# Kernel optimization log

Hardware: AMD Instinct MI355X
Metric: run time of the kernel (lower is better)

## Reference

```python
import jax, jax.numpy as jnp
import numpy as np

B, L = 2, 160
RD = 128          # residue_dim
AD = 128          # atom_dim
NUM_AT = 37       # atom37
NSC = 34          # side-chain atom slots (37 - 3 backbone)
EPS = 8.0         # radius for eps_8 graph
NOISE = 0.5       # noise added to repeated CA positions
HID = 512         # decoder MLP hidden


def _precomputed_atom37_mask():
    # Stand-in for VALID_ATOM37_MASK [20 residue types, 37 atoms]:
    # backbone N,CA,C,O always present; deterministic pseudo side-chain counts.
    m = np.zeros((20, NUM_AT), np.float32)
    m[:, :4] = 1.0
    for r in range(20):
        nsc = 1 + (r * 7) % 10
        m[r, 4:4 + nsc] = 1.0
    return jnp.asarray(m)


def setup_inputs() -> dict:
    key = jax.random.key(0)
    ks = jax.random.split(key, 8)
    bb_pred = jax.random.normal(ks[0], (B, L, 3, 3), jnp.float32) * 10.0
    scalar_features = jax.random.normal(ks[1], (B, L, RD), jnp.float32)
    aa_pred = jax.random.normal(ks[2], (B, L, 20), jnp.float32)
    mask = jnp.ones((B, L), jnp.float32)
    residue_batch = jnp.repeat(jnp.arange(B, dtype=jnp.int64), L)
    # learned parameters
    atom_emb = jax.random.normal(ks[3], (NUM_AT, AD), jnp.float32) * 0.02
    W1 = jax.random.normal(ks[4], (2 * AD, HID), jnp.float32) / np.sqrt(2.0 * AD)
    b1 = jnp.zeros((HID,), jnp.float32)
    W2 = jax.random.normal(ks[5], (HID, 3), jnp.float32) / np.sqrt(float(HID))
    b2 = jnp.zeros((3,), jnp.float32)
    # pre-sampled position noise (torch.randn_like * noise)
    pos_noise = jax.random.normal(ks[6], (B, L, NSC, 3), jnp.float32) * NOISE
    precomputed_mask = _precomputed_atom37_mask()
    return dict(bb_pred=bb_pred, scalar_features=scalar_features, aa_pred=aa_pred,
                residue_batch=residue_batch, mask=mask, precomputed_mask=precomputed_mask,
                atom_emb=atom_emb, W1=W1, b1=b1, W2=W2, b2=b2, pos_noise=pos_noise)


def reference(bb_pred, scalar_features, aa_pred, residue_batch, mask,
              precomputed_mask, atom_emb, W1, b1, W2, b2, pos_noise):
    # --- generate_atom37_mask ---
    res_types = jnp.argmax(aa_pred, axis=-1)                       # [B,L]
    atom_mask = precomputed_mask[res_types] * mask[..., None]      # [B,L,37]

    # --- ResidueAndAtomEmbedder (dense, validity carried as mask) ---
    atom_type_emb = atom_emb[None, None] * atom_mask[..., None]    # [B,L,37,AD]
    combined = scalar_features[:, :, None, :] + atom_type_emb      # [B,L,37,AD]
    sc_mask = atom_mask[:, :, 3:]                                  # [B,L,34]
    h = combined[:, :, 3:, :] * sc_mask[..., None]                 # [B,L,34,AD]

    # --- reconstruct_edges: CA repeated per side-chain slot + noise ---
    ca = bb_pred[:, :, 1, :] * mask[..., None]                     # [B,L,3]
    pos = ca[:, :, None, :] + pos_noise                            # [B,L,34,3]

    Ns = L * NSC
    x = pos.reshape(B, Ns, 3)
    hf = h.reshape(B, Ns, AD)
    valid = sc_mask.reshape(B, Ns)                                 # batch axis B == residue_batch separation

    # pairwise squared distances [B,Ns,Ns] (eps_8 radius graph, dense masked form)
    x2 = jnp.sum(x * x, axis=-1)
    d2 = x2[:, :, None] + x2[:, None, :] - 2.0 * jnp.einsum('bnd,bmd->bnm', x, x)
    pair_valid = valid[:, :, None] * valid[:, None, :]
    w = jnp.where(d2 < EPS * EPS, jnp.exp(-d2 / (2.0 * EPS * EPS)), 0.0) * pair_valid

    # --- PositionDecoder (EGNN-style layer, self-loops contribute zero rel-pos) ---
    deg = jnp.sum(w, axis=-1, keepdims=True)                       # [B,Ns,1]
    inv = 1.0 / (deg + 1.0)
    agg_pos = (x * deg - jnp.einsum('bnm,bmd->bnd', w, x)) * inv   # sum_j w_ij (x_i - x_j), normalized
    h_agg = jnp.einsum('bnm,bmd->bnd', w, hf) * inv                # [B,Ns,AD]
    z = jnp.concatenate([hf, h_agg], axis=-1)                      # [B,Ns,2*AD]
    gate = jnp.tanh(jax.nn.relu(z @ W1 + b1) @ W2 + b2)            # [B,Ns,3]
    disp = agg_pos * gate * valid[..., None]

    updated_pos = (x + disp).reshape(B, L, NSC, 3)
    return atom_mask, updated_pos
```

## Files before the change

### kernel.cpp

```cpp
#include <hip/hip_runtime.h>
#include <hip/hip_bf16.h>
#include <math.h>

#define BB 2
#define LL 160
#define NSC 34
#define NS (LL * NSC)
#define TOT (BB * NS)
#define AD 128
#define ADX 144
#define HID 512
#define NAT 37
#define KC 4
#define NVP 1792
#define NVT 28
#define NVPT (BB * NVP)
#define PEN 1.0e9f

typedef __attribute__((ext_vector_type(4))) float f32x4;
typedef __attribute__((ext_vector_type(8))) short s16x8;
typedef __attribute__((address_space(1))) const unsigned int gu32;
typedef __attribute__((address_space(3))) unsigned int lu32;

__global__ __launch_bounds__(256) void k_pre(
    const float* __restrict__ W1, __hip_bfloat16* __restrict__ W1T,
    const float* __restrict__ bb, const float* __restrict__ aa,
    const float* __restrict__ mask, const float* __restrict__ pm,
    const float* __restrict__ noise,
    float* __restrict__ out_mask, float4* __restrict__ ws_xe,
    float* __restrict__ ws_val, float* __restrict__ out_pos) {
  __shared__ float t[64][65];
  int blk = blockIdx.x;
  int tid = threadIdx.x;
  if (blk < 32) {
    int j0 = (blk >> 2) * 64;
    int c0 = (blk & 3) * 64;
    for (int i = tid; i < 64 * 64; i += 256) {
      int jl = i & 63, cl = i >> 6;
      t[cl][jl] = W1[(size_t)(c0 + cl) * HID + j0 + jl];
    }
    __syncthreads();
    for (int i = tid; i < 64 * 64; i += 256) {
      int cl = i & 63, jl = i >> 6;
      W1T[(size_t)(j0 + jl) * 256 + c0 + cl] = __float2bfloat16(t[cl][jl]);
    }
    return;
  }
  int bl = blk - 32;
  int b = bl / LL, l = bl % LL;
  const float* ap = aa + bl * 20;
  float mv = ap[0]; int rt = 0;
  for (int r = 1; r < 20; ++r) { float v = ap[r]; if (v > mv) { mv = v; rt = r; } }
  float mk = mask[bl];
  const float* pmr = pm + rt * NAT;
  if (tid < NAT) out_mask[bl * NAT + tid] = pmr[tid] * mk;

  float ca0 = bb[(bl * 3 + 1) * 3 + 0] * mk;
  float ca1 = bb[(bl * 3 + 1) * 3 + 1] * mk;
  float ca2 = bb[(bl * 3 + 1) * 3 + 2] * mk;

  if (tid < NSC) {
    float am = pmr[3 + tid] * mk;
    const float* npz = noise + (bl * NSC + tid) * 3;
    float x = ca0 + npz[0], y = ca1 + npz[1], z = ca2 + npz[2];
    float4 xv;
    xv.x = x; xv.y = y; xv.z = z;
    xv.w = x * x + y * y + z * z + (am > 0.f ? 0.f : PEN);
    int g = b * NS + l * NSC + tid;
    ws_xe[g] = xv;
    ws_val[g] = am;
  }
  if (tid < NSC * 3) {
    int s = tid / 3, c = tid % 3;
    float ca = (c == 0) ? ca0 : (c == 1) ? ca1 : ca2;
    float pos = ca + noise[(bl * NSC + s) * 3 + c];
    out_pos[(size_t)(b * NS + l * NSC + s) * 3 + c] = pos;
  }
}

__global__ __launch_bounds__(256) void k_scan(
    const float* __restrict__ ws_val, const float4* __restrict__ ws_xe,
    int* __restrict__ cg2g, float4* __restrict__ xc) {
  __shared__ int scnt[256];
  __shared__ int sincl[256];
  __shared__ int smap[NVP];
  int b = blockIdx.x;
  int tid = threadIdx.x;
  int c = 0;
  if (tid < LL) {
    for (int s = 0; s < NSC; ++s)
      if (ws_val[b * NS + tid * NSC + s] > 0.f) ++c;
  }
  scnt[tid] = c;
  sincl[tid] = c;
  __syncthreads();
  #pragma unroll
  for (int off = 1; off < 256; off <<= 1) {
    int t = (tid >= off) ? sincl[tid - off] : 0;
    __syncthreads();
    sincl[tid] += t;
    __syncthreads();
  }
  for (int j = tid; j < NVP; j += 256) smap[j] = -1;
  __syncthreads();
  if (tid < LL) {
    int o = sincl[tid] - c, k = 0;
    for (int s = 0; s < NSC; ++s) {
      int m = tid * NSC + s;
      if (ws_val[b * NS + m] > 0.f) { smap[o + k] = m; ++k; }
    }
  }
  __syncthreads();
  for (int j = tid; j < NVP; j += 256) {
    int m = smap[j];
    cg2g[b * NVP + j] = m;
    float4 v;
    if (m >= 0) v = ws_xe[b * NS + m];
    else { v.x = 0.f; v.y = 0.f; v.z = 0.f; v.w = PEN; }
    xc[b * NVP + j] = v;
  }
}

__global__ __launch_bounds__(256) void k_prep1c(
    const float* __restrict__ sf, const float* __restrict__ emb,
    const float* __restrict__ ws_val, const int* __restrict__ cg2g,
    const float4* __restrict__ xc, __hip_bfloat16* __restrict__ hfTc,
    __hip_bfloat16* __restrict__ ws_z) {
  __shared__ __hip_bfloat16 tile[ADX][64];
  __shared__ int sm[64];
  int bid = blockIdx.x;
  int b = bid / NVT;
  int j0 = (bid % NVT) * 64;
  int tid = threadIdx.x;
  if (tid < 64) sm[tid] = cg2g[b * NVP + j0 + tid];
  __syncthreads();

  int jl = tid >> 2, cq = tid & 3;
  int m = sm[jl];
  union { s16x8 v[4]; __hip_bfloat16 h[32]; } o;
  if (m >= 0) {
    int l = m / NSC, s = m - l * NSC;
    float am = ws_val[b * NS + m];
    const float* sfp = sf + (size_t)(b * LL + l) * AD + cq * 32;
    const float* emp = emb + (size_t)(3 + s) * AD + cq * 32;
    #pragma unroll 8
    for (int k = 0; k < 32; ++k) {
      float hv = (sfp[k] + emp[k] * am) * am;
      o.h[k] = __float2bfloat16(hv);
      tile[cq * 32 + k][jl] = o.h[k];
    }
  } else {
    __hip_bfloat16 zz = __float2bfloat16(0.0f);
    #pragma unroll 8
    for (int k = 0; k < 32; ++k) { o.h[k] = zz; tile[cq * 32 + k][jl] = zz; }
  }
  {
    __hip_bfloat16* zp = ws_z + ((size_t)(b * NVP + j0 + jl)) * 128 + cq * 32;
    #pragma unroll
    for (int q = 0; q < 4; ++q) *(s16x8*)(zp + q * 8) = o.v[q];
  }
  if (cq == 0) {
    float4 xj = xc[b * NVP + j0 + jl];
    tile[128][jl] = __float2bfloat16(m >= 0 ? 1.0f : 0.0f);
    tile[129][jl] = __float2bfloat16(xj.x);
    tile[130][jl] = __float2bfloat16(xj.y);
    tile[131][jl] = __float2bfloat16(xj.z);
    __hip_bfloat16 zz = __float2bfloat16(0.0f);
    for (int rr = 132; rr < ADX; ++rr) tile[rr][jl] = zz;
  }
  __syncthreads();
  for (int i = tid; i < ADX * 2; i += 256) {
    int r = i >> 1, hf = i & 1;
    __hip_bfloat16* dst = hfTc + (size_t)b * ADX * NVP + (size_t)r * NVP + j0 + hf * 32;
    const __hip_bfloat16* srow = &tile[r][hf * 32];
    #pragma unroll
    for (int q = 0; q < 4; ++q)
      *(s16x8*)(dst + q * 8) = *(const s16x8*)(srow + q * 8);
  }
}

__global__ __launch_bounds__(256, 4) void k_haggc(
    const float4* __restrict__ xc, const __hip_bfloat16* __restrict__ hfTc,
    __hip_bfloat16* __restrict__ haggp, float* __restrict__ dgp) {
  constexpr int NSTEP = NVP / 32;
  constexpr int CH_MAX = (NSTEP + KC - 1) / KC;
  __shared__ float4 xs[(CH_MAX * 4 + 1) * 9];
  __shared__ alignas(16) __hip_bfloat16 sB[2][4608];

  int bid = blockIdx.x;
  int b = bid / (NVT * KC);
  int rem = bid % (NVT * KC);
  int kc = rem / NVT;
  int nt = rem % NVT;
  int n0 = nt * 64;
  int sb = (kc * NSTEP) / KC, se = ((kc + 1) * NSTEP) / KC;
  int tid = threadIdx.x, w = tid >> 6, lane = tid & 63;
  int ln = lane & 15, g8 = (lane >> 4) * 8;

  const float4* xb = xc + b * NVP;
  const __hip_bfloat16* hb = hfTc + (size_t)b * ADX * NVP;

  int mcnt = (se - sb) * 32;
  for (int i = tid; i < mcnt; i += 256)
    xs[(i >> 3) * 9 + (i & 7)] = xb[sb * 32 + i];

  float4 xn = xb[n0 + w * 16 + ln];
  float x2n = xn.w;

  f32x4 acc[9];
  #pragma unroll
  for (int ct = 0; ct < 9; ++ct) acc[ct] = (f32x4){0.f, 0.f, 0.f, 0.f};

  auto STAGE = [&](int s, int pb) {
    const char* srcb = (const char*)(hb + (size_t)s * 32);
    #pragma unroll
    for (int k = 0; k < 3; ++k) {
      int t = tid + k * 256;
      if (t < 576) {
        int row = t >> 2;
        int sl = (t & 3) ^ (row & 3);
        const gu32* gp = (const gu32*)(const void*)(srcb + (size_t)row * (NVP * 2) + sl * 16);
        lu32* lp = (lu32*)(void*)((char*)&sB[pb][0] + (size_t)(t & ~63) * 16);
        __builtin_amdgcn_global_load_lds(gp, lp, 16, 0, 0);
      }
    }
  };

  STAGE(sb, 0);
  __syncthreads();

  int cur = 0;
  for (int s = sb; s < se; ++s) {
    if (s + 1 < se) STAGE(s + 1, cur ^ 1);
    int grp = (s - sb) * 4 + (g8 >> 3);
    union { s16x8 v; __hip_bfloat16 h[8]; } af;
    #pragma unroll
    for (int j = 0; j < 8; ++j) {
      float4 xm = xs[grp * 9 + j];
      float dt = xn.x * xm.x + xn.y * xm.y + xn.z * xm.z;
      float d2 = x2n + xm.w - 2.f * dt;
      float wv = (d2 < 64.f) ? __expf(d2 * -0.0078125f) : 0.f;
      af.h[j] = __float2bfloat16(wv);
    }
    const char* bbase = (const char*)&sB[cur][0];
    int slot = g8 >> 3;
    #pragma unroll
    for (int ct = 0; ct < 9; ++ct) {
      int row = ct * 16 + ln;
      int boff = (row << 6) + ((slot ^ (row & 3)) << 4);
      s16x8 bf = *(const s16x8*)(bbase + boff);
      acc[ct] = __builtin_amdgcn_mfma_f32_16x16x32_bf16(af.v, bf, acc[ct], 0, 0, 0);
    }
    __syncthreads();
    cur ^= 1;
  }

  int q = lane >> 4;
  int grow = b * NVP + n0 + w * 16 + q * 4;
  #pragma unroll
  for (int ct = 0; ct < 8; ++ct)
    #pragma unroll
    for (int r = 0; r < 4; ++r)
      haggp[((size_t)kc * NVPT + grow + r) * AD + ct * 16 + ln] = __float2bfloat16(acc[ct][r]);
  if (ln < 4)
    #pragma unroll
    for (int r = 0; r < 4; ++r)
      dgp[((size_t)kc * NVPT + grow + r) * 4 + ln] = acc[8][r];
}

__global__ __launch_bounds__(512) void k_mlpf(
    const __hip_bfloat16* __restrict__ ws_z,
    const __hip_bfloat16* __restrict__ haggp, const float* __restrict__ dgp,
    const __hip_bfloat16* __restrict__ W1T, const float* __restrict__ b1v,
    const float* __restrict__ W2, const float* __restrict__ b2v,
    const float4* __restrict__ xc, const int* __restrict__ cg2g,
    const float* __restrict__ ws_val, float* __restrict__ out_pos) {
  __shared__ __hip_bfloat16 zt[32][136];
  __shared__ float sai[32][4];
  __shared__ float ppart[4][32][3];

  int r0 = blockIdx.x * 32;
  int tid = threadIdx.x, w = tid >> 6, lane = tid & 63;
  int ln = lane & 15, g8 = (lane >> 4) * 8, q = lane >> 4;
  int rowhalf = w & 1, js4 = w >> 1;

  if (tid < 32) {
    int g = r0 + tid;
    float deg = 0.f, wx = 0.f, wy = 0.f, wz = 0.f;
    #pragma unroll
    for (int kc = 0; kc < KC; ++kc) {
      float4 d = *(const float4*)&dgp[((size_t)kc * NVPT + g) * 4];
      deg += d.x; wx += d.y; wy += d.z; wz += d.w;
    }
    float inv = 1.f / (deg + 1.f);
    float4 xv = xc[g];
    sai[tid][0] = (xv.x * deg - wx) * inv;
    sai[tid][1] = (xv.y * deg - wy) * inv;
    sai[tid][2] = (xv.z * deg - wz) * inv;
    sai[tid][3] = inv;
  }
  __syncthreads();
  {
    int row = tid >> 4, c8 = tid & 15;
    int g = r0 + row;
    float s[8];
    #pragma unroll
    for (int j = 0; j < 8; ++j) s[j] = 0.f;
    #pragma unroll
    for (int kc = 0; kc < KC; ++kc) {
      union { s16x8 v; __hip_bfloat16 h[8]; } uu;
      uu.v = *(const s16x8*)(haggp + ((size_t)kc * NVPT + g) * AD + c8 * 8);
      #pragma unroll
      for (int j = 0; j < 8; ++j) s[j] += __bfloat162float(uu.h[j]);
    }
    float inv = sai[row][3];
    #pragma unroll
    for (int j = 0; j < 8; ++j)
      zt[row][c8 * 8 + j] = __float2bfloat16(s[j] * inv);
  }
  __syncthreads();

  int arl = rowhalf * 16 + ln;
  int arow = r0 + arl;
  s16x8 a[8];
  #pragma unroll
  for (int kq = 0; kq < 4; ++kq)
    a[kq] = *(const s16x8*)(ws_z + (size_t)arow * 128 + kq * 32 + g8);
  #pragma unroll
  for (int kq = 4; kq < 8; ++kq)
    a[kq] = *(const s16x8*)&zt[arl][(kq - 4) * 32 + g8];

  float p[4][3];
  #pragma unroll
  for (int r = 0; r < 4; ++r)
    #pragma unroll
    for (int o = 0; o < 3; ++o) p[r][o] = 0.f;

  #pragma unroll
  for (int jt = 0; jt < 8; ++jt) {
    int j = js4 * 128 + jt * 16 + ln;
    f32x4 acc = (f32x4){0.f, 0.f, 0.f, 0.f};
    #pragma unroll
    for (int kq = 0; kq < 8; ++kq) {
      s16x8 bw = *(const s16x8*)(W1T + (size_t)j * 256 + kq * 32 + g8);
      acc = __builtin_amdgcn_mfma_f32_16x16x32_bf16(a[kq], bw, acc, 0, 0, 0);
    }
    float bias = b1v[j];
    float w20 = W2[j * 3 + 0], w21 = W2[j * 3 + 1], w22 = W2[j * 3 + 2];
    #pragma unroll
    for (int r = 0; r < 4; ++r) {
      float h = fmaxf(acc[r] + bias, 0.f);
      p[r][0] += h * w20; p[r][1] += h * w21; p[r][2] += h * w22;
    }
  }
  #pragma unroll
  for (int r = 0; r < 4; ++r)
    #pragma unroll
    for (int o = 0; o < 3; ++o) {
      p[r][o] += __shfl_xor(p[r][o], 1);
      p[r][o] += __shfl_xor(p[r][o], 2);
      p[r][o] += __shfl_xor(p[r][o], 4);
      p[r][o] += __shfl_xor(p[r][o], 8);
    }
  if (ln == 0) {
    #pragma unroll
    for (int r = 0; r < 4; ++r) {
      int row = rowhalf * 16 + q * 4 + r;
      #pragma unroll
      for (int o = 0; o < 3; ++o) ppart[js4][row][o] = p[r][o];
    }
  }
  __syncthreads();

  if (tid < 32) {
    int row = tid;
    int g = r0 + row;
    int bq = g / NVP;
    int m = cg2g[g];
    if (m >= 0) {
      float p0 = b2v[0] + ppart[0][row][0] + ppart[1][row][0] + ppart[2][row][0] + ppart[3][row][0];
      float p1 = b2v[1] + ppart[0][row][1] + ppart[1][row][1] + ppart[2][row][1] + ppart[3][row][1];
      float p2 = b2v[2] + ppart[0][row][2] + ppart[1][row][2] + ppart[2][row][2] + ppart[3][row][2];
      float val = ws_val[bq * NS + m];
      float4 xv = xc[g];
      float* op = out_pos + (size_t)(bq * NS + m) * 3;
      op[0] = xv.x + sai[row][0] * tanhf(p0) * val;
      op[1] = xv.y + sai[row][1] * tanhf(p1) * val;
      op[2] = xv.z + sai[row][2] * tanhf(p2) * val;
    }
  }
}

extern "C" void kernel_launch(void* const* d_in, const int* in_sizes, int n_in,
                              void* d_out, int out_size, void* d_ws, size_t ws_size,
                              hipStream_t stream) {
  const float* bb    = (const float*)d_in[0];
  const float* sf    = (const float*)d_in[1];
  const float* aa    = (const float*)d_in[2];
  const float* mask  = (const float*)d_in[4];
  const float* pm    = (const float*)d_in[5];
  const float* emb   = (const float*)d_in[6];
  const float* W1    = (const float*)d_in[7];
  const float* b1v   = (const float*)d_in[8];
  const float* W2    = (const float*)d_in[9];
  const float* b2v   = (const float*)d_in[10];
  const float* noise = (const float*)d_in[11];

  float* out_mask = (float*)d_out;
  float* out_pos  = (float*)d_out + BB * LL * NAT;

  char* cur = (char*)d_ws;
  auto alloc = [&](size_t bytes) -> char* {
    char* p = cur;
    cur += (bytes + 15) & ~(size_t)15;
    return p;
  };
  float4* ws_xe  = (float4*)alloc((size_t)TOT * 16);
  float*  ws_val = (float*)alloc((size_t)TOT * 4);
  int*    cg2g   = (int*)alloc((size_t)BB * NVP * 4);
  float4* xc     = (float4*)alloc((size_t)BB * NVP * 16);
  float*  ws_dgp = (float*)alloc((size_t)KC * NVPT * 16);
  __hip_bfloat16* ws_w1t = (__hip_bfloat16*)alloc((size_t)HID * 256 * 2);
  __hip_bfloat16* hfTc   = (__hip_bfloat16*)alloc((size_t)BB * ADX * NVP * 2);
  __hip_bfloat16* haggp  = (__hip_bfloat16*)alloc((size_t)KC * NVPT * AD * 2);
  __hip_bfloat16* ws_z   = (__hip_bfloat16*)alloc((size_t)NVPT * 128 * 2);

  hipLaunchKernelGGL(k_pre, dim3(32 + BB * LL), dim3(256), 0, stream,
                     W1, ws_w1t, bb, aa, mask, pm, noise,
                     out_mask, ws_xe, ws_val, out_pos);
  hipLaunchKernelGGL(k_scan, dim3(BB), dim3(256), 0, stream,
                     ws_val, ws_xe, cg2g, xc);
  hipLaunchKernelGGL(k_prep1c, dim3(BB * NVT), dim3(256), 0, stream,
                     sf, emb, ws_val, cg2g, xc, hfTc, ws_z);
  hipLaunchKernelGGL(k_haggc, dim3(BB * NVT * KC), dim3(256), 0, stream,
                     xc, hfTc, haggp, ws_dgp);
  hipLaunchKernelGGL(k_mlpf, dim3(NVPT / 32), dim3(512), 0, stream,
                     ws_z, haggp, ws_dgp, ws_w1t, b1v, W2, b2v,
                     xc, cg2g, ws_val, out_pos);
}
```

Measured before the change: 58.90 us.

## Fuse five kernels into one persistent kernel with global grid barriers

```diff
diff --git a/kernel.cpp b/kernel.cpp
--- a/kernel.cpp
+++ b/kernel.cpp
@@ -15,6 +15,7 @@
 #define NVP 1792
 #define NVT 28
 #define NVPT (BB * NVP)
+#define NBLK 224
 #define PEN 1.0e9f
 
 typedef __attribute__((ext_vector_type(4))) float f32x4;
@@ -22,371 +23,374 @@
 typedef __attribute__((address_space(1))) const unsigned int gu32;
 typedef __attribute__((address_space(3))) unsigned int lu32;
 
-__global__ __launch_bounds__(256) void k_pre(
-    const float* __restrict__ W1, __hip_bfloat16* __restrict__ W1T,
-    const float* __restrict__ bb, const float* __restrict__ aa,
-    const float* __restrict__ mask, const float* __restrict__ pm,
-    const float* __restrict__ noise,
-    float* __restrict__ out_mask, float4* __restrict__ ws_xe,
-    float* __restrict__ ws_val, float* __restrict__ out_pos) {
-  __shared__ float t[64][65];
-  int blk = blockIdx.x;
+__device__ __forceinline__ void gbar(int* bar, int idx) {
+  __syncthreads();
+  if (threadIdx.x == 0) {
+    __threadfence();
+    int* cnt = bar + idx * 2;
+    int* flg = bar + idx * 2 + 1;
+    if (atomicAdd(cnt, 1) == NBLK - 1) {
+      atomicExch(flg, 1);
+    } else {
+      while (atomicAdd(flg, 0) == 0) __builtin_amdgcn_s_sleep(2);
+    }
+    __threadfence();
+  }
+  __syncthreads();
+}
+
+struct LdsP0 { float t[64][65]; };
+struct LdsP1 { int scnt[256]; int sincl[256]; int smap[NVP]; };
+struct LdsP2 { __hip_bfloat16 tile[ADX][64]; int sm[64]; };
+struct LdsP3 { float4 xs[57 * 9]; __hip_bfloat16 sB[2][4608]; };
+struct LdsP4 { __hip_bfloat16 zt[16][136]; float sai[16][4]; float ppart[4][16][3]; };
+
+__global__ __launch_bounds__(256) void k_mega(
+    const float* __restrict__ W1, const float* __restrict__ bb,
+    const float* __restrict__ aa, const float* __restrict__ mask,
+    const float* __restrict__ pm, const float* __restrict__ noise,
+    const float* __restrict__ sf, const float* __restrict__ emb,
+    const float* __restrict__ b1v, const float* __restrict__ W2,
+    const float* __restrict__ b2v,
+    float* __restrict__ out_mask, float* __restrict__ out_pos,
+    __hip_bfloat16* __restrict__ W1T, float4* __restrict__ ws_xe,
+    float* __restrict__ ws_val, int* __restrict__ cg2g,
+    float4* __restrict__ xc, __hip_bfloat16* __restrict__ hfTc,
+    __hip_bfloat16* __restrict__ ws_z, __hip_bfloat16* __restrict__ haggp,
+    float* __restrict__ dgp, int* bar) {
+  __shared__ union { LdsP0 p0; LdsP1 p1; LdsP2 p2; LdsP3 p3; LdsP4 p4; } u;
   int tid = threadIdx.x;
-  if (blk < 32) {
-    int j0 = (blk >> 2) * 64;
-    int c0 = (blk & 3) * 64;
-    for (int i = tid; i < 64 * 64; i += 256) {
-      int jl = i & 63, cl = i >> 6;
-      t[cl][jl] = W1[(size_t)(c0 + cl) * HID + j0 + jl];
-    }
-    __syncthreads();
-    for (int i = tid; i < 64 * 64; i += 256) {
-      int cl = i & 63, jl = i >> 6;
-      W1T[(size_t)(j0 + jl) * 256 + c0 + cl] = __float2bfloat16(t[cl][jl]);
-    }
-    return;
-  }
-  int bl = blk - 32;
-  int b = bl / LL, l = bl % LL;
-  const float* ap = aa + bl * 20;
-  float mv = ap[0]; int rt = 0;
-  for (int r = 1; r < 20; ++r) { float v = ap[r]; if (v > mv) { mv = v; rt = r; } }
-  float mk = mask[bl];
-  const float* pmr = pm + rt * NAT;
-  if (tid < NAT) out_mask[bl * NAT + tid] = pmr[tid] * mk;
-
-  float ca0 = bb[(bl * 3 + 1) * 3 + 0] * mk;
-  float ca1 = bb[(bl * 3 + 1) * 3 + 1] * mk;
-  float ca2 = bb[(bl * 3 + 1) * 3 + 2] * mk;
-
-  if (tid < NSC) {
-    float am = pmr[3 + tid] * mk;
-    const float* npz = noise + (bl * NSC + tid) * 3;
-    float x = ca0 + npz[0], y = ca1 + npz[1], z = ca2 + npz[2];
-    float4 xv;
-    xv.x = x; xv.y = y; xv.z = z;
-    xv.w = x * x + y * y + z * z + (am > 0.f ? 0.f : PEN);
-    int g = b * NS + l * NSC + tid;
-    ws_xe[g] = xv;
-    ws_val[g] = am;
-  }
-  if (tid < NSC * 3) {
-    int s = tid / 3, c = tid % 3;
-    float ca = (c == 0) ? ca0 : (c == 1) ? ca1 : ca2;
-    float pos = ca + noise[(bl * NSC + s) * 3 + c];
-    out_pos[(size_t)(b * NS + l * NSC + s) * 3 + c] = pos;
-  }
-}
-
-__global__ __launch_bounds__(256) void k_scan(
-    const float* __restrict__ ws_val, const float4* __restrict__ ws_xe,
-    int* __restrict__ cg2g, float4* __restrict__ xc) {
-  __shared__ int scnt[256];
-  __shared__ int sincl[256];
-  __shared__ int smap[NVP];
-  int b = blockIdx.x;
-  int tid = threadIdx.x;
-  int c = 0;
-  if (tid < LL) {
-    for (int s = 0; s < NSC; ++s)
-      if (ws_val[b * NS + tid * NSC + s] > 0.f) ++c;
-  }
-  scnt[tid] = c;
-  sincl[tid] = c;
-  __syncthreads();
-  #pragma unroll
-  for (int off = 1; off < 256; off <<= 1) {
-    int t = (tid >= off) ? sincl[tid - off] : 0;
-    __syncthreads();
-    sincl[tid] += t;
-    __syncthreads();
-  }
-  for (int j = tid; j < NVP; j += 256) smap[j] = -1;
-  __syncthreads();
-  if (tid < LL) {
-    int o = sincl[tid] - c, k = 0;
-    for (int s = 0; s < NSC; ++s) {
-      int m = tid * NSC + s;
-      if (ws_val[b * NS + m] > 0.f) { smap[o + k] = m; ++k; }
-    }
-  }
-  __syncthreads();
-  for (int j = tid; j < NVP; j += 256) {
-    int m = smap[j];
-    cg2g[b * NVP + j] = m;
-    float4 v;
-    if (m >= 0) v = ws_xe[b * NS + m];
-    else { v.x = 0.f; v.y = 0.f; v.z = 0.f; v.w = PEN; }
-    xc[b * NVP + j] = v;
-  }
-}
-
-__global__ __launch_bounds__(256) void k_prep1c(
-    const float* __restrict__ sf, const float* __restrict__ emb,
-    const float* __restrict__ ws_val, const int* __restrict__ cg2g,
-    const float4* __restrict__ xc, __hip_bfloat16* __restrict__ hfTc,
-    __hip_bfloat16* __restrict__ ws_z) {
-  __shared__ __hip_bfloat16 tile[ADX][64];
-  __shared__ int sm[64];
-  int bid = blockIdx.x;
-  int b = bid / NVT;
-  int j0 = (bid % NVT) * 64;
-  int tid = threadIdx.x;
-  if (tid < 64) sm[tid] = cg2g[b * NVP + j0 + tid];
-  __syncthreads();
-
-  int jl = tid >> 2, cq = tid & 3;
-  int m = sm[jl];
-  union { s16x8 v[4]; __hip_bfloat16 h[32]; } o;
-  if (m >= 0) {
-    int l = m / NSC, s = m - l * NSC;
-    float am = ws_val[b * NS + m];
-    const float* sfp = sf + (size_t)(b * LL + l) * AD + cq * 32;
-    const float* emp = emb + (size_t)(3 + s) * AD + cq * 32;
-    #pragma unroll 8
-    for (int k = 0; k < 32; ++k) {
-      float hv = (sfp[k] + emp[k] * am) * am;
-      o.h[k] = __float2bfloat16(hv);
-      tile[cq * 32 + k][jl] = o.h[k];
-    }
-  } else {
-    __hip_bfloat16 zz = __float2bfloat16(0.0f);
-    #pragma unroll 8
-    for (int k = 0; k < 32; ++k) { o.h[k] = zz; tile[cq * 32 + k][jl] = zz; }
-  }
+
+  for (int v = blockIdx.x; v < 32 + BB * LL; v += NBLK) {
+    if (v < 32) {
+      int j0 = (v >> 2) * 64, c0 = (v & 3) * 64;
+      for (int i = tid; i < 64 * 64; i += 256) {
+        int jl = i & 63, cl = i >> 6;
+        u.p0.t[cl][jl] = W1[(size_t)(c0 + cl) * HID + j0 + jl];
+      }
+      __syncthreads();
+      for (int i = tid; i < 64 * 64; i += 256) {
+        int cl = i & 63, jl = i >> 6;
+        W1T[(size_t)(j0 + jl) * 256 + c0 + cl] = __float2bfloat16(u.p0.t[cl][jl]);
+      }
+    } else {
+      int bl = v - 32;
+      int b = bl / LL, l = bl % LL;
+      const float* ap = aa + bl * 20;
+      float mv = ap[0]; int rt = 0;
+      for (int r = 1; r < 20; ++r) { float vv = ap[r]; if (vv > mv) { mv = vv; rt = r; } }
+      float mk = mask[bl];
+      const float* pmr = pm + rt * NAT;
+      if (tid < NAT) out_mask[bl * NAT + tid] = pmr[tid] * mk;
+
+      float ca0 = bb[(bl * 3 + 1) * 3 + 0] * mk;
+      float ca1 = bb[(bl * 3 + 1) * 3 + 1] * mk;
+      float ca2 = bb[(bl * 3 + 1) * 3 + 2] * mk;
+
+      if (tid < NSC) {
+        float am = pmr[3 + tid] * mk;
+        const float* npz = noise + (bl * NSC + tid) * 3;
+        float x = ca0 + npz[0], y = ca1 + npz[1], z = ca2 + npz[2];
+        float4 xv;
+        xv.x = x; xv.y = y; xv.z = z;
+        xv.w = x * x + y * y + z * z + (am > 0.f ? 0.f : PEN);
+        int g = b * NS + l * NSC + tid;
+        ws_xe[g] = xv;
+        ws_val[g] = am;
+      }
+      if (tid < NSC * 3) {
+        int s = tid / 3, c = tid % 3;
+        float ca = (c == 0) ? ca0 : (c == 1) ? ca1 : ca2;
+        float pos = ca + noise[(bl * NSC + s) * 3 + c];
+        out_pos[(size_t)(b * NS + l * NSC + s) * 3 + c] = pos;
+      }
+    }
+    __syncthreads();
+  }
+  gbar(bar, 0);
+
+  if (blockIdx.x < BB) {
+    int b = blockIdx.x;
+    int c = 0;
+    if (tid < LL) {
+      for (int s = 0; s < NSC; ++s)
+        if (ws_val[b * NS + tid * NSC + s] > 0.f) ++c;
+    }
+    u.p1.scnt[tid] = c;
+    u.p1.sincl[tid] = c;
+    __syncthreads();
+    #pragma unroll
+    for (int off = 1; off < 256; off <<= 1) {
+      int t = (tid >= off) ? u.p1.sincl[tid - off] : 0;
+      __syncthreads();
+      u.p1.sincl[tid] += t;
+      __syncthreads();
+    }
+    for (int j = tid; j < NVP; j += 256) u.p1.smap[j] = -1;
+    __syncthreads();
+    if (tid < LL) {
+      int o = u.p1.sincl[tid] - c, k = 0;
+      for (int s = 0; s < NSC; ++s) {
+        int m = tid * NSC + s;
+        if (ws_val[b * NS + m] > 0.f) { u.p1.smap[o + k] = m; ++k; }
+      }
+    }
+    __syncthreads();
+    for (int j = tid; j < NVP; j += 256) {
+      int m = u.p1.smap[j];
+      cg2g[b * NVP + j] = m;
+      float4 vv;
+      if (m >= 0) vv = ws_xe[b * NS + m];
+      else { vv.x = 0.f; vv.y = 0.f; vv.z = 0.f; vv.w = PEN; }
+      xc[b * NVP + j] = vv;
+    }
+  }
+  gbar(bar, 1);
+
+  if (blockIdx.x < BB * NVT) {
+    int bid = blockIdx.x;
+    int b = bid / NVT;
+    int j0 = (bid % NVT) * 64;
+    if (tid < 64) u.p2.sm[tid] = cg2g[b * NVP + j0 + tid];
+    __syncthreads();
+
+    int jl = tid >> 2, cq = tid & 3;
+    int m = u.p2.sm[jl];
+    union { s16x8 v[4]; __hip_bfloat16 h[32]; } o;
+    if (m >= 0) {
+      int l = m / NSC, s = m - l * NSC;
+      float am = ws_val[b * NS + m];
+      const float* sfp = sf + (size_t)(b * LL + l) * AD + cq * 32;
+      const float* emp = emb + (size_t)(3 + s) * AD + cq * 32;
+      #pragma unroll 8
+      for (int k = 0; k < 32; ++k) {
+        float hv = (sfp[k] + emp[k] * am) * am;
+        o.h[k] = __float2bfloat16(hv);
+        u.p2.tile[cq * 32 + k][jl] = o.h[k];
+      }
+    } else {
+      __hip_bfloat16 zz = __float2bfloat16(0.0f);
+      #pragma unroll 8
+      for (int k = 0; k < 32; ++k) { o.h[k] = zz; u.p2.tile[cq * 32 + k][jl] = zz; }
+    }
+    {
+      __hip_bfloat16* zp = ws_z + ((size_t)(b * NVP + j0 + jl)) * 128 + cq * 32;
+      #pragma unroll
+      for (int q = 0; q < 4; ++q) *(s16x8*)(zp + q * 8) = o.v[q];
+    }
+    if (cq == 0) {
+      float4 xj = xc[b * NVP + j0 + jl];
+      u.p2.tile[128][jl] = __float2bfloat16(m >= 0 ? 1.0f : 0.0f);
+      u.p2.tile[129][jl] = __float2bfloat16(xj.x);
+      u.p2.tile[130][jl] = __float2bfloat16(xj.y);
+      u.p2.tile[131][jl] = __float2bfloat16(xj.z);
+      __hip_bfloat16 zz = __float2bfloat16(0.0f);
+      for (int rr = 132; rr < ADX; ++rr) u.p2.tile[rr][jl] = zz;
+    }
+    __syncthreads();
+    for (int i = tid; i < ADX * 2; i += 256) {
+      int r = i >> 1, hf = i & 1;
+      __hip_bfloat16* dst = hfTc + (size_t)b * ADX * NVP + (size_t)r * NVP + j0 + hf * 32;
+      const __hip_bfloat16* srow = &u.p2.tile[r][hf * 32];
+      #pragma unroll
+      for (int q = 0; q < 4; ++q)
+        *(s16x8*)(dst + q * 8) = *(const s16x8*)(srow + q * 8);
+    }
+  }
+  gbar(bar, 2);
+
   {
-    __hip_bfloat16* zp = ws_z + ((size_t)(b * NVP + j0 + jl)) * 128 + cq * 32;
-    #pragma unroll
-    for (int q = 0; q < 4; ++q) *(s16x8*)(zp + q * 8) = o.v[q];
-  }
-  if (cq == 0) {
-    float4 xj = xc[b * NVP + j0 + jl];
-    tile[128][jl] = __float2bfloat16(m >= 0 ? 1.0f : 0.0f);
-    tile[129][jl] = __float2bfloat16(xj.x);
-    tile[130][jl] = __float2bfloat16(xj.y);
-    tile[131][jl] = __float2bfloat16(xj.z);
-    __hip_bfloat16 zz = __float2bfloat16(0.0f);
-    for (int rr = 132; rr < ADX; ++rr) tile[rr][jl] = zz;
-  }
-  __syncthreads();
-  for (int i = tid; i < ADX * 2; i += 256) {
-    int r = i >> 1, hf = i & 1;
-    __hip_bfloat16* dst = hfTc + (size_t)b * ADX * NVP + (size_t)r * NVP + j0 + hf * 32;
-    const __hip_bfloat16* srow = &tile[r][hf * 32];
-    #pragma unroll
-    for (int q = 0; q < 4; ++q)
-      *(s16x8*)(dst + q * 8) = *(const s16x8*)(srow + q * 8);
-  }
-}
-
-__global__ __launch_bounds__(256, 4) void k_haggc(
-    const float4* __restrict__ xc, const __hip_bfloat16* __restrict__ hfTc,
-    __hip_bfloat16* __restrict__ haggp, float* __restrict__ dgp) {
-  constexpr int NSTEP = NVP / 32;
-  constexpr int CH_MAX = (NSTEP + KC - 1) / KC;
-  __shared__ float4 xs[(CH_MAX * 4 + 1) * 9];
-  __shared__ alignas(16) __hip_bfloat16 sB[2][4608];
-
-  int bid = blockIdx.x;
-  int b = bid / (NVT * KC);
-  int rem = bid % (NVT * KC);
-  int kc = rem / NVT;
-  int nt = rem % NVT;
-  int n0 = nt * 64;
-  int sb = (kc * NSTEP) / KC, se = ((kc + 1) * NSTEP) / KC;
-  int tid = threadIdx.x, w = tid >> 6, lane = tid & 63;
-  int ln = lane & 15, g8 = (lane >> 4) * 8;
-
-  const float4* xb = xc + b * NVP;
-  const __hip_bfloat16* hb = hfTc + (size_t)b * ADX * NVP;
-
-  int mcnt = (se - sb) * 32;
-  for (int i = tid; i < mcnt; i += 256)
-    xs[(i >> 3) * 9 + (i & 7)] = xb[sb * 32 + i];
-
-  float4 xn = xb[n0 + w * 16 + ln];
-  float x2n = xn.w;
-
-  f32x4 acc[9];
-  #pragma unroll
-  for (int ct = 0; ct < 9; ++ct) acc[ct] = (f32x4){0.f, 0.f, 0.f, 0.f};
-
-  auto STAGE = [&](int s, int pb) {
-    const char* srcb = (const char*)(hb + (size_t)s * 32);
-    #pragma unroll
-    for (int k = 0; k < 3; ++k) {
-      int t = tid + k * 256;
-      if (t < 576) {
-        int row = t >> 2;
-        int sl = (t & 3) ^ (row & 3);
-        const gu32* gp = (const gu32*)(const void*)(srcb + (size_t)row * (NVP * 2) + sl * 16);
-        lu32* lp = (lu32*)(void*)((char*)&sB[pb][0] + (size_t)(t & ~63) * 16);
-        __builtin_amdgcn_global_load_lds(gp, lp, 16, 0, 0);
-      }
-    }
-  };
-
-  STAGE(sb, 0);
-  __syncthreads();
-
-  int cur = 0;
-  for (int s = sb; s < se; ++s) {
-    if (s + 1 < se) STAGE(s + 1, cur ^ 1);
-    int grp = (s - sb) * 4 + (g8 >> 3);
-    union { s16x8 v; __hip_bfloat16 h[8]; } af;
-    #pragma unroll
-    for (int j = 0; j < 8; ++j) {
-      float4 xm = xs[grp * 9 + j];
-      float dt = xn.x * xm.x + xn.y * xm.y + xn.z * xm.z;
-      float d2 = x2n + xm.w - 2.f * dt;
-      float wv = (d2 < 64.f) ? __expf(d2 * -0.0078125f) : 0.f;
-      af.h[j] = __float2bfloat16(wv);
-    }
-    const char* bbase = (const char*)&sB[cur][0];
-    int slot = g8 >> 3;
-    #pragma unroll
-    for (int ct = 0; ct < 9; ++ct) {
-      int row = ct * 16 + ln;
-      int boff = (row << 6) + ((slot ^ (row & 3)) << 4);
-      s16x8 bf = *(const s16x8*)(bbase + boff);
-      acc[ct] = __builtin_amdgcn_mfma_f32_16x16x32_bf16(af.v, bf, acc[ct], 0, 0, 0);
-    }
-    __syncthreads();
-    cur ^= 1;
-  }
-
-  int q = lane >> 4;
-  int grow = b * NVP + n0 + w * 16 + q * 4;
-  #pragma unroll
-  for (int ct = 0; ct < 8; ++ct)
+    constexpr int NSTEP = NVP / 32;
+    int bid = blockIdx.x;
+    int b = bid / (NVT * KC);
+    int rem = bid % (NVT * KC);
+    int kc = rem / NVT;
+    int nt = rem % NVT;
+    int n0 = nt * 64;
+    int sb = (kc * NSTEP) / KC, se = ((kc + 1) * NSTEP) / KC;
+    int w = tid >> 6, lane = tid & 63;
+    int ln = lane & 15, g8 = (lane >> 4) * 8;
+
+    const float4* xb = xc + b * NVP;
+    const __hip_bfloat16* hb = hfTc + (size_t)b * ADX * NVP;
+
+    int mcnt = (se - sb) * 32;
+    for (int i = tid; i < mcnt; i += 256)
+      u.p3.xs[(i >> 3) * 9 + (i & 7)] = xb[sb * 32 + i];
+
+    float4 xn = xb[n0 + w * 16 + ln];
+    float x2n = xn.w;
+
+    f32x4 acc[9];
+    #pragma unroll
+    for (int ct = 0; ct < 9; ++ct) acc[ct] = (f32x4){0.f, 0.f, 0.f, 0.f};
+
+    auto STAGE = [&](int s, int pb) {
+      const char* srcb = (const char*)(hb + (size_t)s * 32);
+      #pragma unroll
+      for (int k = 0; k < 3; ++k) {
+        int t = tid + k * 256;
+        if (t < 576) {
+          int row = t >> 2;
+          int sl = (t & 3) ^ (row & 3);
+          const gu32* gp = (const gu32*)(const void*)(srcb + (size_t)row * (NVP * 2) + sl * 16);
+          lu32* lp = (lu32*)(void*)((char*)&u.p3.sB[pb][0] + (size_t)(t & ~63) * 16);
+          __builtin_amdgcn_global_load_lds(gp, lp, 16, 0, 0);
+        }
+      }
+    };
+
+    STAGE(sb, 0);
+    __syncthreads();
+
+    int cur = 0;
+    for (int s = sb; s < se; ++s) {
+      if (s + 1 < se) STAGE(s + 1, cur ^ 1);
+      int grp = (s - sb) * 4 + (g8 >> 3);
+      union { s16x8 v; __hip_bfloat16 h[8]; } af;
+      #pragma unroll
+      for (int j = 0; j < 8; ++j) {
+        float4 xm = u.p3.xs[grp * 9 + j];
+        float dt = xn.x * xm.x + xn.y * xm.y + xn.z * xm.z;
+        float d2 = x2n + xm.w - 2.f * dt;
+        float wv = (d2 < 64.f) ? __expf(d2 * -0.0078125f) : 0.f;
+        af.h[j] = __float2bfloat16(wv);
+      }
+      const char* bbase = (const char*)&u.p3.sB[cur][0];
+      int slot = g8 >> 3;
+      #pragma unroll
+      for (int ct = 0; ct < 9; ++ct) {
+        int row = ct * 16 + ln;
+        int boff = (row << 6) + ((slot ^ (row & 3)) << 4);
+        s16x8 bf = *(const s16x8*)(bbase + boff);
+        acc[ct] = __builtin_amdgcn_mfma_f32_16x16x32_bf16(af.v, bf, acc[ct], 0, 0, 0);
+      }
+      __syncthreads();
+      cur ^= 1;
+    }
+
+    int q = lane >> 4;
+    int grow = b * NVP + n0 + w * 16 + q * 4;
+    #pragma unroll
+    for (int ct = 0; ct < 8; ++ct)
+      #pragma unroll
+      for (int r = 0; r < 4; ++r)
+        haggp[((size_t)kc * NVPT + grow + r) * AD + ct * 16 + ln] = __float2bfloat16(acc[ct][r]);
+    if (ln < 4)
+      #pragma unroll
+      for (int r = 0; r < 4; ++r)
+        dgp[((size_t)kc * NVPT + grow + r) * 4 + ln] = acc[8][r];
+  }
+  gbar(bar, 3);
+
+  {
+    int r0 = blockIdx.x * 16;
+    int w = tid >> 6, lane = tid & 63;
+    int ln = lane & 15, g8 = (lane >> 4) * 8, q = lane >> 4;
+
+    if (tid < 16) {
+      int g = r0 + tid;
+      float deg = 0.f, wx = 0.f, wy = 0.f, wz = 0.f;
+      #pragma unroll
+      for (int kc = 0; kc < KC; ++kc) {
+        float4 d = *(const float4*)&dgp[((size_t)kc * NVPT + g) * 4];
+        deg += d.x; wx += d.y; wy += d.z; wz += d.w;
+      }
+      float inv = 1.f / (deg + 1.f);
+      float4 xv = xc[g];
+      u.p4.sai[tid][0] = (xv.x * deg - wx) * inv;
+      u.p4.sai[tid][1] = (xv.y * deg - wy) * inv;
+      u.p4.sai[tid][2] = (xv.z * deg - wz) * inv;
+      u.p4.sai[tid][3] = inv;
+    }
+    __syncthreads();
+    {
+      int row = tid >> 4, c8 = tid & 15;
+      int g = r0 + row;
+      float s[8];
+      #pragma unroll
+      for (int j = 0; j < 8; ++j) s[j] = 0.f;
+      #pragma unroll
+      for (int kc = 0; kc < KC; ++kc) {
+        union { s16x8 v; __hip_bfloat16 h[8]; } uu;
+        uu.v = *(const s16x8*)(haggp + ((size_t)kc * NVPT + g) * AD + c8 * 8);
+        #pragma unroll
+        for (int j = 0; j < 8; ++j) s[j] += __bfloat162float(uu.h[j]);
+      }
+      float inv = u.p4.sai[row][3];
+      #pragma unroll
+      for (int j = 0; j < 8; ++j)
+        u.p4.zt[row][c8 * 8 + j] = __float2bfloat16(s[j] * inv);
+    }
+    __syncthreads();
+
+    int arow = r0 + ln;
+    s16x8 a[8];
+    #pragma unroll
+    for (int kq = 0; kq < 4; ++kq)
+      a[kq] = *(const s16x8*)(ws_z + (size_t)arow * 128 + kq * 32 + g8);
+    #pragma unroll
+    for (int kq = 4; kq < 8; ++kq)
+      a[kq] = *(const s16x8*)&u.p4.zt[ln][(kq - 4) * 32 + g8];
+
+    float p[4][3];
     #pragma unroll
     for (int r = 0; r < 4; ++r)
-      haggp[((size_t)kc * NVPT + grow + r) * AD + ct * 16 + ln] = __float2bfloat16(acc[ct][r]);
-  if (ln < 4)
+      #pragma unroll
+      for (int o = 0; o < 3; ++o) p[r][o] = 0.f;
+
+    #pragma unroll
+    for (int jt = 0; jt < 8; ++jt) {
+      int j = w * 128 + jt * 16 + ln;
+      f32x4 acc = (f32x4){0.f, 0.f, 0.f, 0.f};
+      #pragma unroll
+      for (int kq = 0; kq < 8; ++kq) {
+        s16x8 bw = *(const s16x8*)(W1T + (size_t)j * 256 + kq * 32 + g8);
+        acc = __builtin_amdgcn_mfma_f32_16x16x32_bf16(a[kq], bw, acc, 0, 0, 0);
+      }
+      float bias = b1v[j];
+      float w20 = W2[j * 3 + 0], w21 = W2[j * 3 + 1], w22 = W2[j * 3 + 2];
+      #pragma unroll
+      for (int r = 0; r < 4; ++r) {
+        float h = fmaxf(acc[r] + bias, 0.f);
+        p[r][0] += h * w20; p[r][1] += h * w21; p[r][2] += h * w22;
+      }
+    }
     #pragma unroll
     for (int r = 0; r < 4; ++r)
-      dgp[((size_t)kc * NVPT + grow + r) * 4 + ln] = acc[8][r];
-}
-
-__global__ __launch_bounds__(512) void k_mlpf(
-    const __hip_bfloat16* __restrict__ ws_z,
-    const __hip_bfloat16* __restrict__ haggp, const float* __restrict__ dgp,
-    const __hip_bfloat16* __restrict__ W1T, const float* __restrict__ b1v,
-    const float* __restrict__ W2, const float* __restrict__ b2v,
-    const float4* __restrict__ xc, const int* __restrict__ cg2g,
-    const float* __restrict__ ws_val, float* __restrict__ out_pos) {
-  __shared__ __hip_bfloat16 zt[32][136];
-  __shared__ float sai[32][4];
-  __shared__ float ppart[4][32][3];
-
-  int r0 = blockIdx.x * 32;
-  int tid = threadIdx.x, w = tid >> 6, lane = tid & 63;
-  int ln = lane & 15, g8 = (lane >> 4) * 8, q = lane >> 4;
-  int rowhalf = w & 1, js4 = w >> 1;
-
-  if (tid < 32) {
-    int g = r0 + tid;
-    float deg = 0.f, wx = 0.f, wy = 0.f, wz = 0.f;
-    #pragma unroll
-    for (int kc = 0; kc < KC; ++kc) {
-      float4 d = *(const float4*)&dgp[((size_t)kc * NVPT + g) * 4];
-      deg += d.x; wx += d.y; wy += d.z; wz += d.w;
-    }
-    float inv = 1.f / (deg + 1.f);
-    float4 xv = xc[g];
-    sai[tid][0] = (xv.x * deg - wx) * inv;
-    sai[tid][1] = (xv.y * deg - wy) * inv;
-    sai[tid][2] = (xv.z * deg - wz) * inv;
-    sai[tid][3] = inv;
-  }
-  __syncthreads();
-  {
-    int row = tid >> 4, c8 = tid & 15;
-    int g = r0 + row;
-    float s[8];
-    #pragma unroll
-    for (int j = 0; j < 8; ++j) s[j] = 0.f;
-    #pragma unroll
-    for (int kc = 0; kc < KC; ++kc) {
-      union { s16x8 v; __hip_bfloat16 h[8]; } uu;
-      uu.v = *(const s16x8*)(haggp + ((size_t)kc * NVPT + g) * AD + c8 * 8);
-      #pragma unroll
-      for (int j = 0; j < 8; ++j) s[j] += __bfloat162float(uu.h[j]);
-    }
-    float inv = sai[row][3];
-    #pragma unroll
-    for (int j = 0; j < 8; ++j)
-      zt[row][c8 * 8 + j] = __float2bfloat16(s[j] * inv);
-  }
-  __syncthreads();
-
-  int arl = rowhalf * 16 + ln;
-  int arow = r0 + arl;
-  s16x8 a[8];
-  #pragma unroll
-  for (int kq = 0; kq < 4; ++kq)
-    a[kq] = *(const s16x8*)(ws_z + (size_t)arow * 128 + kq * 32 + g8);
-  #pragma unroll
-  for (int kq = 4; kq < 8; ++kq)
-    a[kq] = *(const s16x8*)&zt[arl][(kq - 4) * 32 + g8];
-
-  float p[4][3];
-  #pragma unroll
-  for (int r = 0; r < 4; ++r)
-    #pragma unroll
-    for (int o = 0; o < 3; ++o) p[r][o] = 0.f;
-
-  #pragma unroll
-  for (int jt = 0; jt < 8; ++jt) {
-    int j = js4 * 128 + jt * 16 + ln;
-    f32x4 acc = (f32x4){0.f, 0.f, 0.f, 0.f};
-    #pragma unroll
-    for (int kq = 0; kq < 8; ++kq) {
-      s16x8 bw = *(const s16x8*)(W1T + (size_t)j * 256 + kq * 32 + g8);
-      acc = __builtin_amdgcn_mfma_f32_16x16x32_bf16(a[kq], bw, acc, 0, 0, 0);
-    }
-    float bias = b1v[j];
-    float w20 = W2[j * 3 + 0], w21 = W2[j * 3 + 1], w22 = W2[j * 3 + 2];
-    #pragma unroll
-    for (int r = 0; r < 4; ++r) {
-      float h = fmaxf(acc[r] + bias, 0.f);
-      p[r][0] += h * w20; p[r][1] += h * w21; p[r][2] += h * w22;
-    }
-  }
-  #pragma unroll
-  for (int r = 0; r < 4; ++r)
-    #pragma unroll
-    for (int o = 0; o < 3; ++o) {
-      p[r][o] += __shfl_xor(p[r][o], 1);
-      p[r][o] += __shfl_xor(p[r][o], 2);
-      p[r][o] += __shfl_xor(p[r][o], 4);
-      p[r][o] += __shfl_xor(p[r][o], 8);
-    }
-  if (ln == 0) {
-    #pragma unroll
-    for (int r = 0; r < 4; ++r) {
-      int row = rowhalf * 16 + q * 4 + r;
-      #pragma unroll
-      for (int o = 0; o < 3; ++o) ppart[js4][row][o] = p[r][o];
-    }
-  }
-  __syncthreads();
-
-  if (tid < 32) {
-    int row = tid;
-    int g = r0 + row;
-    int bq = g / NVP;
-    int m = cg2g[g];
-    if (m >= 0) {
-      float p0 = b2v[0] + ppart[0][row][0] + ppart[1][row][0] + ppart[2][row][0] + ppart[3][row][0];
-      float p1 = b2v[1] + ppart[0][row][1] + ppart[1][row][1] + ppart[2][row][1] + ppart[3][row][1];
-      float p2 = b2v[2] + ppart[0][row][2] + ppart[1][row][2] + ppart[2][row][2] + ppart[3][row][2];
-      float val = ws_val[bq * NS + m];
-      float4 xv = xc[g];
-      float* op = out_pos + (size_t)(bq * NS + m) * 3;
-      op[0] = xv.x + sai[row][0] * tanhf(p0) * val;
-      op[1] = xv.y + sai[row][1] * tanhf(p1) * val;
-      op[2] = xv.z + sai[row][2] * tanhf(p2) * val;
+      #pragma unroll
+      for (int o = 0; o < 3; ++o) {
+        p[r][o] += __shfl_xor(p[r][o], 1);
+        p[r][o] += __shfl_xor(p[r][o], 2);
+        p[r][o] += __shfl_xor(p[r][o], 4);
+        p[r][o] += __shfl_xor(p[r][o], 8);
+      }
+    if (ln == 0) {
+      #pragma unroll
+      for (int r = 0; r < 4; ++r) {
+        int row = q * 4 + r;
+        #pragma unroll
+        for (int o = 0; o < 3; ++o) u.p4.ppart[w][row][o] = p[r][o];
+      }
+    }
+    __syncthreads();
+
+    if (tid < 16) {
+      int row = tid;
+      int g = r0 + row;
+      int bq = g / NVP;
+      int m = cg2g[g];
+      if (m >= 0) {
+        float p0 = b2v[0] + u.p4.ppart[0][row][0] + u.p4.ppart[1][row][0] + u.p4.ppart[2][row][0] + u.p4.ppart[3][row][0];
+        float p1 = b2v[1] + u.p4.ppart[0][row][1] + u.p4.ppart[1][row][1] + u.p4.ppart[2][row][1] + u.p4.ppart[3][row][1];
+        float p2 = b2v[2] + u.p4.ppart[0][row][2] + u.p4.ppart[1][row][2] + u.p4.ppart[2][row][2] + u.p4.ppart[3][row][2];
+        float val = ws_val[bq * NS + m];
+        float4 xv = xc[g];
+        float* op = out_pos + (size_t)(bq * NS + m) * 3;
+        op[0] = xv.x + u.p4.sai[row][0] * tanhf(p0) * val;
+        op[1] = xv.y + u.p4.sai[row][1] * tanhf(p1) * val;
+        op[2] = xv.z + u.p4.sai[row][2] * tanhf(p2) * val;
+      }
     }
   }
 }
@@ -415,6 +419,7 @@
     cur += (bytes + 15) & ~(size_t)15;
     return p;
   };
+  int*    bar    = (int*)alloc(64);
   float4* ws_xe  = (float4*)alloc((size_t)TOT * 16);
   float*  ws_val = (float*)alloc((size_t)TOT * 4);
   int*    cg2g   = (int*)alloc((size_t)BB * NVP * 4);
@@ -425,16 +430,9 @@
   __hip_bfloat16* haggp  = (__hip_bfloat16*)alloc((size_t)KC * NVPT * AD * 2);
   __hip_bfloat16* ws_z   = (__hip_bfloat16*)alloc((size_t)NVPT * 128 * 2);
 
-  hipLaunchKernelGGL(k_pre, dim3(32 + BB * LL), dim3(256), 0, stream,
-                     W1, ws_w1t, bb, aa, mask, pm, noise,
-                     out_mask, ws_xe, ws_val, out_pos);
-  hipLaunchKernelGGL(k_scan, dim3(BB), dim3(256), 0, stream,
-                     ws_val, ws_xe, cg2g, xc);
-  hipLaunchKernelGGL(k_prep1c, dim3(BB * NVT), dim3(256), 0, stream,
-                     sf, emb, ws_val, cg2g, xc, hfTc, ws_z);
-  hipLaunchKernelGGL(k_haggc, dim3(BB * NVT * KC), dim3(256), 0, stream,
-                     xc, hfTc, haggp, ws_dgp);
-  hipLaunchKernelGGL(k_mlpf, dim3(NVPT / 32), dim3(512), 0, stream,
-                     ws_z, haggp, ws_dgp, ws_w1t, b1v, W2, b2v,
-                     xc, cg2g, ws_val, out_pos);
+  hipMemsetAsync(bar, 0, 64, stream);
+  hipLaunchKernelGGL(k_mega, dim3(NBLK), dim3(256), 0, stream,
+                     W1, bb, aa, mask, pm, noise, sf, emb, b1v, W2, b2v,
+                     out_mask, out_pos, ws_w1t, ws_xe, ws_val, cg2g, xc,
+                     hfTc, ws_z, haggp, ws_dgp, bar);
 }
```

Result: slower. 117.3 us (+99.1%).

## Fuse compaction scan into prep kernel and double neighbor-chunk split

Applied to the files above, without the earlier changes.

```diff
diff --git a/kernel.cpp b/kernel.cpp
--- a/kernel.cpp
+++ b/kernel.cpp
@@ -11,7 +11,7 @@
 #define ADX 144
 #define HID 512
 #define NAT 37
-#define KC 4
+#define KC 8
 #define NVP 1792
 #define NVT 28
 #define NVPT (BB * NVP)
@@ -78,20 +78,24 @@
   }
 }
 
-__global__ __launch_bounds__(256) void k_scan(
+__global__ __launch_bounds__(256) void k_prep1c(
+    const float* __restrict__ sf, const float* __restrict__ emb,
     const float* __restrict__ ws_val, const float4* __restrict__ ws_xe,
-    int* __restrict__ cg2g, float4* __restrict__ xc) {
-  __shared__ int scnt[256];
+    int* __restrict__ cg2g, float4* __restrict__ xc,
+    __hip_bfloat16* __restrict__ hfTc, __hip_bfloat16* __restrict__ ws_z) {
   __shared__ int sincl[256];
   __shared__ int smap[NVP];
-  int b = blockIdx.x;
+  __shared__ __hip_bfloat16 tile[ADX][64];
+  int bid = blockIdx.x;
+  int b = bid / NVT;
+  int j0 = (bid % NVT) * 64;
   int tid = threadIdx.x;
+
   int c = 0;
   if (tid < LL) {
     for (int s = 0; s < NSC; ++s)
       if (ws_val[b * NS + tid * NSC + s] > 0.f) ++c;
   }
-  scnt[tid] = c;
   sincl[tid] = c;
   __syncthreads();
   #pragma unroll
@@ -111,7 +115,9 @@
     }
   }
   __syncthreads();
-  for (int j = tid; j < NVP; j += 256) {
+
+  if (tid < 64) {
+    int j = j0 + tid;
     int m = smap[j];
     cg2g[b * NVP + j] = m;
     float4 v;
@@ -119,24 +125,9 @@
     else { v.x = 0.f; v.y = 0.f; v.z = 0.f; v.w = PEN; }
     xc[b * NVP + j] = v;
   }
-}
-
-__global__ __launch_bounds__(256) void k_prep1c(
-    const float* __restrict__ sf, const float* __restrict__ emb,
-    const float* __restrict__ ws_val, const int* __restrict__ cg2g,
-    const float4* __restrict__ xc, __hip_bfloat16* __restrict__ hfTc,
-    __hip_bfloat16* __restrict__ ws_z) {
-  __shared__ __hip_bfloat16 tile[ADX][64];
-  __shared__ int sm[64];
-  int bid = blockIdx.x;
-  int b = bid / NVT;
-  int j0 = (bid % NVT) * 64;
-  int tid = threadIdx.x;
-  if (tid < 64) sm[tid] = cg2g[b * NVP + j0 + tid];
-  __syncthreads();
 
   int jl = tid >> 2, cq = tid & 3;
-  int m = sm[jl];
+  int m = smap[j0 + jl];
   union { s16x8 v[4]; __hip_bfloat16 h[32]; } o;
   if (m >= 0) {
     int l = m / NSC, s = m - l * NSC;
@@ -160,11 +151,15 @@
     for (int q = 0; q < 4; ++q) *(s16x8*)(zp + q * 8) = o.v[q];
   }
   if (cq == 0) {
-    float4 xj = xc[b * NVP + j0 + jl];
+    float xjx = 0.f, xjy = 0.f, xjz = 0.f;
+    if (m >= 0) {
+      float4 xj = ws_xe[b * NS + m];
+      xjx = xj.x; xjy = xj.y; xjz = xj.z;
+    }
     tile[128][jl] = __float2bfloat16(m >= 0 ? 1.0f : 0.0f);
-    tile[129][jl] = __float2bfloat16(xj.x);
-    tile[130][jl] = __float2bfloat16(xj.y);
-    tile[131][jl] = __float2bfloat16(xj.z);
+    tile[129][jl] = __float2bfloat16(xjx);
+    tile[130][jl] = __float2bfloat16(xjy);
+    tile[131][jl] = __float2bfloat16(xjz);
     __hip_bfloat16 zz = __float2bfloat16(0.0f);
     for (int rr = 132; rr < ADX; ++rr) tile[rr][jl] = zz;
   }
@@ -412,7 +407,7 @@
   char* cur = (char*)d_ws;
   auto alloc = [&](size_t bytes) -> char* {
     char* p = cur;
-    cur += (bytes + 15) & ~(size_t)15;
+    cur += (bytes + 255) & ~(size_t)255;
     return p;
   };
   float4* ws_xe  = (float4*)alloc((size_t)TOT * 16);
@@ -428,10 +423,8 @@
   hipLaunchKernelGGL(k_pre, dim3(32 + BB * LL), dim3(256), 0, stream,
                      W1, ws_w1t, bb, aa, mask, pm, noise,
                      out_mask, ws_xe, ws_val, out_pos);
-  hipLaunchKernelGGL(k_scan, dim3(BB), dim3(256), 0, stream,
-                     ws_val, ws_xe, cg2g, xc);
   hipLaunchKernelGGL(k_prep1c, dim3(BB * NVT), dim3(256), 0, stream,
-                     sf, emb, ws_val, cg2g, xc, hfTc, ws_z);
+                     sf, emb, ws_val, ws_xe, cg2g, xc, hfTc, ws_z);
   hipLaunchKernelGGL(k_haggc, dim3(BB * NVT * KC), dim3(256), 0, stream,
                      xc, hfTc, haggp, ws_dgp);
   hipLaunchKernelGGL(k_mlpf, dim3(NVPT / 32), dim3(512), 0, stream,
```

Result: faster. 53.75 us (-8.8%).
